# Performance work log

Measured on AMD Instinct MI355X. Metric: run time of the kernel, lower is better.

Reference implementation:

```python
import jax, jax.numpy as jnp
import numpy as np

B, S, D = 4, 2048, 1024
H = 16
HD = D // H          # 64
HALF = HD // 2       # 32


def _rope(t, cos, sin):
    # t: [B, S, H, HD]; cos/sin: [S, HALF]
    tr = t.reshape(*t.shape[:-1], HALF, 2)
    t0, t1 = tr[..., 0], tr[..., 1]
    c = cos[None, :, None, :]
    s = sin[None, :, None, :]
    out = jnp.stack([t0 * c - t1 * s, t0 * s + t1 * c], axis=-1)
    return out.reshape(t.shape)


def setup_inputs() -> dict:
    key = jax.random.key(0)
    ks = jax.random.split(key, 7)
    x = jax.random.normal(ks[0], (B, S, D), dtype=jnp.float32)
    # rotary tables (theta=10000 convention)
    inv_freq = 1.0 / (10000.0 ** (np.arange(0, HD, 2, dtype=np.float32) / HD))
    angles = np.arange(S, dtype=np.float32)[:, None] * inv_freq[None, :]
    freqs_cos = jnp.asarray(np.cos(angles))
    freqs_sin = jnp.asarray(np.sin(angles))
    scale = 1.0 / np.sqrt(D)
    wq = jax.random.normal(ks[1], (D, D), dtype=jnp.float32) * scale
    wk = jax.random.normal(ks[2], (D, D), dtype=jnp.float32) * scale
    wv = jax.random.normal(ks[3], (D, D), dtype=jnp.float32) * scale
    wo = jax.random.normal(ks[4], (D, D), dtype=jnp.float32) * scale
    return {"x": x, "freqs_cos": freqs_cos, "freqs_sin": freqs_sin,
            "wq": wq, "wk": wk, "wv": wv, "wo": wo}


def reference(x, freqs_cos, freqs_sin, wq, wk, wv, wo):
    b, s, d = x.shape
    q = (x @ wq.T).reshape(b, s, H, HD)
    k = (x @ wk.T).reshape(b, s, H, HD)
    v = (x @ wv.T).reshape(b, s, H, HD)
    q = _rope(q, freqs_cos, freqs_sin)
    k = _rope(k, freqs_cos, freqs_sin)
    # [B, H, S, HD]
    q = q.transpose(0, 2, 1, 3)
    k = k.transpose(0, 2, 1, 3)
    v = v.transpose(0, 2, 1, 3)
    scores = jnp.einsum("bhqd,bhkd->bhqk", q, k) / jnp.sqrt(jnp.float32(HD))
    causal = jnp.tril(jnp.ones((s, s), dtype=bool))
    scores = jnp.where(causal[None, None, :, :], scores, jnp.finfo(scores.dtype).min)
    attn = jax.nn.softmax(scores, axis=-1)
    out = jnp.einsum("bhqk,bhkd->bhqd", attn, v)
    out = out.transpose(0, 2, 1, 3).reshape(b, s, d)
    return out @ wo.T
```

## Files before the change

### kernel.cpp

```cpp
#include <hip/hip_runtime.h>
#include <hip/hip_bf16.h>
#include <cstdint>
#include <cstddef>

#define BB 4
#define SS 2048
#define DD 1024
#define HH 16
#define HDD 64

typedef __bf16 bf16_t;
typedef __bf16 bf16x8 __attribute__((ext_vector_type(8)));
typedef float f32x4 __attribute__((ext_vector_type(4)));
typedef unsigned u32x2 __attribute__((ext_vector_type(2)));

__device__ __forceinline__ unsigned short f2bf(float f) {
    unsigned u = __float_as_uint(f);
    unsigned r = (u + 0x7FFFu + ((u >> 16) & 1u)) >> 16;
    return (unsigned short)r;
}
__device__ __forceinline__ bf16_t f2bf16(float f) {
    return __builtin_bit_cast(bf16_t, f2bf(f));
}
__device__ __forceinline__ bf16x8 cvt8(float4 a, float4 b) {
    bf16x8 r;
    r[0] = f2bf16(a.x); r[1] = f2bf16(a.y);
    r[2] = f2bf16(a.z); r[3] = f2bf16(a.w);
    r[4] = f2bf16(b.x); r[5] = f2bf16(b.y);
    r[6] = f2bf16(b.z); r[7] = f2bf16(b.w);
    return r;
}
__device__ __forceinline__ unsigned cvtpk_bf16(float lo, float hi) {
    unsigned r;
    asm("v_cvt_pk_bf16_f32 %0, %1, %2" : "=v"(r) : "v"(lo), "v"(hi));
    return r;
}
__device__ __forceinline__ float exp2_raw(float x) {
    float r;
    asm("v_exp_f32 %0, %1" : "=v"(r) : "v"(x));
    return r;
}

#define GLL16(gp, lp)                                                          \
    __builtin_amdgcn_global_load_lds(                                          \
        (const __attribute__((address_space(1))) void*)(gp),                   \
        (__attribute__((address_space(3))) void*)(lp), 16, 0, 0)

__global__ __launch_bounds__(256) void cvt1(const float* __restrict__ in,
                                            bf16_t* __restrict__ out) {
    size_t i = (size_t)blockIdx.x * 256 + threadIdx.x;
    const float4* p = (const float4*)in + i * 2;
    *(bf16x8*)(out + i * 8) = cvt8(p[0], p[1]);
}
__global__ __launch_bounds__(256) void cvt4(
    const float* __restrict__ w0, const float* __restrict__ w1,
    const float* __restrict__ w2, const float* __restrict__ w3,
    bf16_t* __restrict__ o0, bf16_t* __restrict__ o1,
    bf16_t* __restrict__ o2, bf16_t* __restrict__ o3) {
    const float* in = blockIdx.y == 0 ? w0 : blockIdx.y == 1 ? w1
                    : blockIdx.y == 2 ? w2 : w3;
    bf16_t* out = blockIdx.y == 0 ? o0 : blockIdx.y == 1 ? o1
                : blockIdx.y == 2 ? o2 : o3;
    size_t i = (size_t)blockIdx.x * 256 + threadIdx.x;
    const float4* p = (const float4*)in + i * 2;
    *(bf16x8*)(out + i * 8) = cvt8(p[0], p[1]);
}

__global__ __launch_bounds__(256, 2) void gemm_qkv(
    const bf16_t* __restrict__ A, const bf16_t* __restrict__ Wall,
    bf16_t* __restrict__ Qb, bf16_t* __restrict__ Kb,
    bf16_t* __restrict__ Vt,
    const float* __restrict__ fcos, const float* __restrict__ fsin,
    float qscale)
{
    constexpr int K = 1024;
    __shared__ alignas(16) bf16_t lA[128 * 64];
    __shared__ alignas(16) bf16_t lB[128 * 64];

    const int tid  = threadIdx.x;
    const int w    = tid >> 6;
    const int lane = tid & 63;
    const int quad = lane >> 4;
    const int l16  = lane & 15;
    const int wm   = w >> 1;
    const int wn   = w & 1;
    const int m0   = blockIdx.y * 128;
    const int n0   = blockIdx.x * 128;
    const int sub  = n0 >> 10;

    f32x4 acc[4][4];
#pragma unroll
    for (int i = 0; i < 4; i++)
#pragma unroll
        for (int j = 0; j < 4; j++) acc[i][j] = (f32x4){0.f, 0.f, 0.f, 0.f};

    const int srow8 = lane >> 3;
    const int slot  = lane & 7;

    for (int k0 = 0; k0 < K; k0 += 64) {
#pragma unroll
        for (int i = 0; i < 4; ++i) {
            int row = w * 32 + i * 8;
            GLL16(A + (size_t)(m0 + row + srow8) * K + k0 + slot * 8,
                  &lA[row * 64]);
            GLL16(Wall + (size_t)(n0 + row + srow8) * K + k0 + slot * 8,
                  &lB[row * 64]);
        }
        __syncthreads();
#pragma unroll
        for (int kk = 0; kk < 2; ++kk) {
            bf16x8 af[4], bfr[4];
#pragma unroll
            for (int mt = 0; mt < 4; ++mt)
                af[mt] = *(const bf16x8*)
                    &lA[(wm * 64 + mt * 16 + l16) * 64 + (kk * 4 + quad) * 8];
#pragma unroll
            for (int nt = 0; nt < 4; ++nt)
                bfr[nt] = *(const bf16x8*)
                    &lB[(wn * 64 + nt * 16 + l16) * 64 + (kk * 4 + quad) * 8];
#pragma unroll
            for (int mt = 0; mt < 4; ++mt)
#pragma unroll
                for (int nt = 0; nt < 4; ++nt)
                    acc[mt][nt] = __builtin_amdgcn_mfma_f32_16x16x32_bf16(
                        af[mt], bfr[nt], acc[mt][nt], 0, 0, 0);
        }
        __syncthreads();
    }

    if (sub < 2) {
        unsigned short* Cu = (unsigned short*)(sub == 0 ? Qb : Kb);
        const float scale = sub == 0 ? qscale : 1.0f;
#pragma unroll
        for (int mt = 0; mt < 4; ++mt) {
#pragma unroll
            for (int nt = 0; nt < 4; ++nt) {
                int col  = (n0 & 1023) + wn * 64 + nt * 16 + l16;
                int h    = col >> 6;
                int d    = col & 63;
                int pidx = d >> 1;
                bool even = (col & 1) == 0;
#pragma unroll
                for (int r = 0; r < 4; ++r) {
                    int m = m0 + wm * 64 + mt * 16 + quad * 4 + r;
                    int b = m >> 11;
                    int s = m & 2047;
                    float v  = acc[mt][nt][r];
                    float p  = __shfl_xor(v, 1);
                    float c  = fcos[s * 32 + pidx];
                    float sn = fsin[s * 32 + pidx];
                    float o  = even ? (v * c - p * sn) : (p * sn + v * c);
                    Cu[(size_t)((b * HH + h) * SS + s) * HDD + d] =
                        f2bf(o * scale);
                }
            }
        }
    } else {
        unsigned short* Cu = (unsigned short*)Vt;
#pragma unroll
        for (int mt = 0; mt < 4; ++mt) {
#pragma unroll
            for (int nt = 0; nt < 4; ++nt) {
                int col = (n0 & 1023) + wn * 64 + nt * 16 + l16;
                int h = col >> 6, d = col & 63;
#pragma unroll
                for (int r = 0; r < 4; ++r) {
                    int m = m0 + wm * 64 + mt * 16 + quad * 4 + r;
                    int b = m >> 11, s = m & 2047;
                    Cu[(size_t)((b * HH + h) * HDD + d) * SS + s] =
                        f2bf(acc[mt][nt][r]);
                }
            }
        }
    }
}

__global__ __launch_bounds__(256, 2) void gemm_out(
    const bf16_t* __restrict__ A, const bf16_t* __restrict__ W,
    float* __restrict__ Cf)
{
    constexpr int K = 1024, N = 1024;
    __shared__ alignas(16) bf16_t lA[128 * 64];
    __shared__ alignas(16) bf16_t lB[128 * 64];

    const int tid  = threadIdx.x;
    const int w    = tid >> 6;
    const int lane = tid & 63;
    const int quad = lane >> 4;
    const int l16  = lane & 15;
    const int wm   = w >> 1;
    const int wn   = w & 1;
    const int m0   = blockIdx.y * 128;
    const int n0   = blockIdx.x * 128;

    f32x4 acc[4][4];
#pragma unroll
    for (int i = 0; i < 4; i++)
#pragma unroll
        for (int j = 0; j < 4; j++) acc[i][j] = (f32x4){0.f, 0.f, 0.f, 0.f};

    const int srow8 = lane >> 3;
    const int slot  = lane & 7;

    for (int k0 = 0; k0 < K; k0 += 64) {
#pragma unroll
        for (int i = 0; i < 4; ++i) {
            int row = w * 32 + i * 8;
            GLL16(A + (size_t)(m0 + row + srow8) * K + k0 + slot * 8,
                  &lA[row * 64]);
            GLL16(W + (size_t)(n0 + row + srow8) * K + k0 + slot * 8,
                  &lB[row * 64]);
        }
        __syncthreads();
#pragma unroll
        for (int kk = 0; kk < 2; ++kk) {
            bf16x8 af[4], bfr[4];
#pragma unroll
            for (int mt = 0; mt < 4; ++mt)
                af[mt] = *(const bf16x8*)
                    &lA[(wm * 64 + mt * 16 + l16) * 64 + (kk * 4 + quad) * 8];
#pragma unroll
            for (int nt = 0; nt < 4; ++nt)
                bfr[nt] = *(const bf16x8*)
                    &lB[(wn * 64 + nt * 16 + l16) * 64 + (kk * 4 + quad) * 8];
#pragma unroll
            for (int mt = 0; mt < 4; ++mt)
#pragma unroll
                for (int nt = 0; nt < 4; ++nt)
                    acc[mt][nt] = __builtin_amdgcn_mfma_f32_16x16x32_bf16(
                        af[mt], bfr[nt], acc[mt][nt], 0, 0, 0);
        }
        __syncthreads();
    }

#pragma unroll
    for (int mt = 0; mt < 4; ++mt) {
        int mrow = m0 + wm * 64 + mt * 16 + quad * 4;
#pragma unroll
        for (int nt = 0; nt < 4; ++nt) {
            int col = n0 + wn * 64 + nt * 16 + l16;
#pragma unroll
            for (int r = 0; r < 4; ++r)
                Cf[(size_t)(mrow + r) * N + col] = acc[mt][nt][r];
        }
    }
}

__global__ __launch_bounds__(256, 2) void attn(
    const bf16_t* __restrict__ Q, const bf16_t* __restrict__ Kt,
    const bf16_t* __restrict__ Vt, bf16_t* __restrict__ O)
{
    __shared__ alignas(16) bf16_t lK[64 * 64];
    __shared__ alignas(16) bf16_t lV[64 * 64];

    const int tid  = threadIdx.x;
    const int w    = tid >> 6;
    const int lane = tid & 63;
    const int quad = lane >> 4;
    const int l16  = lane & 15;

    const int blk  = blockIdx.x;
    const int xcd  = blk & 7;
    const int rest = blk >> 3;
    const int j    = rest & 15;
    const int bh   = ((rest >> 4) << 3) | xcd;
    const int T    = (j & 1) ? (j >> 1) : (15 - (j >> 1));

    const int b = bh >> 4, h = bh & 15;
    unsigned short* Ou = (unsigned short*)O;
    const bf16_t* Qb = Q  + (size_t)bh * SS * HDD;
    const bf16_t* Kb = Kt + (size_t)bh * SS * HDD;
    const bf16_t* Vb = Vt + (size_t)bh * HDD * SS;

    const int r0a = w * 16;
    const int r0b = w * 16 + 8;
    const int rra = r0a + (lane >> 3);
    const int rrb = r0b + (lane >> 3);
    const int sca = ((lane & 7) ^ (rra & 7)) * 8;
    const int scb = ((lane & 7) ^ (rrb & 7)) * 8;

    const int q0  = T * 128 + w * 32;
    const int nkb = 2 * T + 2;

    bf16x8 qf[2][2];
#pragma unroll
    for (int qs = 0; qs < 2; ++qs) {
        const bf16_t* qp =
            Qb + (size_t)(q0 + qs * 16 + l16) * HDD + quad * 8;
        qf[qs][0] = *(const bf16x8*)(qp);
        qf[qs][1] = *(const bf16x8*)(qp + 32);
    }

    f32x4 o[2][4];
    float ps[2];
#pragma unroll
    for (int qs = 0; qs < 2; ++qs) {
        ps[qs] = 0.f;
#pragma unroll
        for (int i = 0; i < 4; ++i) o[qs][i] = (f32x4){0.f, 0.f, 0.f, 0.f};
    }

    for (int ib = 0; ib < nkb; ++ib) {
        const int kb = ib * 64;

        GLL16(Kb + (size_t)(kb + rra) * HDD + sca, &lK[r0a * 64]);
        GLL16(Kb + (size_t)(kb + rrb) * HDD + scb, &lK[r0b * 64]);
        GLL16(Vb + (size_t)rra * SS + kb + sca,    &lV[r0a * 64]);
        GLL16(Vb + (size_t)rrb * SS + kb + scb,    &lV[r0b * 64]);
        __syncthreads();

        if (kb < q0 + 32) {
            const bool diag = (kb + 63 > q0);

            bf16x8 kf[4][2];
#pragma unroll
            for (int nt = 0; nt < 4; ++nt) {
                const int row = nt * 16 + l16;
#pragma unroll
                for (int hf = 0; hf < 2; ++hf)
                    kf[nt][hf] = *(const bf16x8*)
                        &lK[row * 64 + (((hf * 4 + quad) ^ (row & 7)) * 8)];
            }
            bf16x8 vf[2][4];
#pragma unroll
            for (int kk = 0; kk < 2; ++kk)
#pragma unroll
                for (int nt = 0; nt < 4; ++nt) {
                    const int row = nt * 16 + l16;
                    vf[kk][nt] = *(const bf16x8*)
                        &lV[row * 64 + (((kk * 4 + quad) ^ (row & 7)) * 8)];
                }

            unsigned pk[4][2][2];
#pragma unroll
            for (int nt = 0; nt < 4; ++nt) {
                const int krow = kb + nt * 16 + quad * 4;
#pragma unroll
                for (int qs = 0; qs < 2; ++qs) {
                    f32x4 s = (f32x4){0.f, 0.f, 0.f, 0.f};
                    s = __builtin_amdgcn_mfma_f32_16x16x32_bf16(
                        kf[nt][0], qf[qs][0], s, 0, 0, 0);
                    s = __builtin_amdgcn_mfma_f32_16x16x32_bf16(
                        kf[nt][1], qf[qs][1], s, 0, 0, 0);
                    if (diag) {
                        const int qcol = q0 + qs * 16 + l16;
#pragma unroll
                        for (int r = 0; r < 4; ++r)
                            if (krow + r > qcol) s[r] = -1e30f;
                    }
                    float ev[4];
#pragma unroll
                    for (int r = 0; r < 4; ++r) {
                        float e = exp2_raw(s[r]);
                        ps[qs] += e;
                        ev[r] = e;
                    }
                    pk[nt][qs][0] = cvtpk_bf16(ev[0], ev[1]);
                    pk[nt][qs][1] = cvtpk_bf16(ev[2], ev[3]);
                }
            }

#pragma unroll
            for (int kk = 0; kk < 2; ++kk) {
#pragma unroll
                for (int qs = 0; qs < 2; ++qs) {
                    u32x2 sA = __builtin_amdgcn_permlane32_swap(
                        pk[2 * kk][qs][0], pk[2 * kk + 1][qs][0],
                        false, false);
                    u32x2 sB = __builtin_amdgcn_permlane32_swap(
                        pk[2 * kk][qs][1], pk[2 * kk + 1][qs][1],
                        false, false);
                    u32x2 tA = __builtin_amdgcn_permlane16_swap(
                        sA.x, sA.y, false, false);
                    u32x2 tB = __builtin_amdgcn_permlane16_swap(
                        sB.x, sB.y, false, false);
                    union { unsigned d[4]; bf16x8 v; } pf;
                    pf.d[0] = tA.x;
                    pf.d[1] = tB.x;
                    pf.d[2] = tA.y;
                    pf.d[3] = tB.y;
#pragma unroll
                    for (int nt = 0; nt < 4; ++nt)
                        o[qs][nt] = __builtin_amdgcn_mfma_f32_16x16x32_bf16(
                            pf.v, vf[kk][nt], o[qs][nt], 0, 0, 0);
                }
            }
        }
        __syncthreads();
    }

#pragma unroll
    for (int qs = 0; qs < 2; ++qs) {
        float tsum = ps[qs];
        tsum += __shfl_xor(tsum, 16);
        tsum += __shfl_xor(tsum, 32);
        float inv[4];
#pragma unroll
        for (int r = 0; r < 4; ++r)
            inv[r] = 1.0f / __shfl(tsum, quad * 4 + r);
#pragma unroll
        for (int nt = 0; nt < 4; ++nt) {
            int d = nt * 16 + l16;
#pragma unroll
            for (int r = 0; r < 4; ++r) {
                int s = q0 + qs * 16 + quad * 4 + r;
                Ou[(size_t)(b * SS + s) * DD + h * HDD + d] =
                    f2bf(o[qs][nt][r] * inv[r]);
            }
        }
    }
}

extern "C" void kernel_launch(void* const* d_in, const int* in_sizes, int n_in,
                              void* d_out, int out_size, void* d_ws,
                              size_t ws_size, hipStream_t stream)
{
    const float* x    = (const float*)d_in[0];
    const float* fcos = (const float*)d_in[1];
    const float* fsin = (const float*)d_in[2];
    const float* wq   = (const float*)d_in[3];
    const float* wk   = (const float*)d_in[4];
    const float* wv   = (const float*)d_in[5];
    const float* wo   = (const float*)d_in[6];

    char* ws = (char*)d_ws;
    const size_t TSZ = (size_t)BB * SS * DD * sizeof(bf16_t);
    const size_t WSZ = (size_t)DD * DD * sizeof(bf16_t);
    bf16_t* Qb  = (bf16_t*)(ws);
    bf16_t* Kb  = (bf16_t*)(ws + TSZ);
    bf16_t* Ob  = (bf16_t*)(ws + 2 * TSZ);
    bf16_t* wb0 = (bf16_t*)(ws + 3 * TSZ);
    bf16_t* wb1 = (bf16_t*)(ws + 3 * TSZ + WSZ);
    bf16_t* wb2 = (bf16_t*)(ws + 3 * TSZ + 2 * WSZ);
    bf16_t* wb3 = (bf16_t*)(ws + 3 * TSZ + 3 * WSZ);
    bf16_t* xb  = (bf16_t*)d_out;
    bf16_t* Vt  = (bf16_t*)((char*)d_out + TSZ);

    dim3 bb(256);
    cvt1<<<dim3(4096), bb, 0, stream>>>(x, xb);
    cvt4<<<dim3(512, 4), bb, 0, stream>>>(wq, wk, wv, wo, wb0, wb1, wb2, wb3);

    const float sscale = 0.125f * 1.44269504088896f;
    gemm_qkv<<<dim3(24, 64), bb, 0, stream>>>(xb, wb0, Qb, Kb, Vt,
                                              fcos, fsin, sscale);
    attn<<<dim3(1024), bb, 0, stream>>>(Qb, Kb, Vt, Ob);
    gemm_out<<<dim3(8, 64), bb, 0, stream>>>(Ob, wb3, (float*)d_out);
}
```

Baseline: 276.8 us.

## Double-buffer LDS tiles in output GEMM and attention K/V loops

Measured after the change: 279.8 us. About the same (+1.1%).

```diff
diff --git a/kernel.cpp b/kernel.cpp
--- a/kernel.cpp
+++ b/kernel.cpp
@@ -180,8 +180,8 @@
     float* __restrict__ Cf)
 {
     constexpr int K = 1024, N = 1024;
-    __shared__ alignas(16) bf16_t lA[128 * 64];
-    __shared__ alignas(16) bf16_t lB[128 * 64];
+    __shared__ alignas(16) bf16_t lA[2][128 * 64];
+    __shared__ alignas(16) bf16_t lB[2][128 * 64];
 
     const int tid  = threadIdx.x;
     const int w    = tid >> 6;
@@ -202,27 +202,34 @@
     const int srow8 = lane >> 3;
     const int slot  = lane & 7;
 
-    for (int k0 = 0; k0 < K; k0 += 64) {
+    auto stage = [&](int k0, int buf) {
 #pragma unroll
         for (int i = 0; i < 4; ++i) {
             int row = w * 32 + i * 8;
             GLL16(A + (size_t)(m0 + row + srow8) * K + k0 + slot * 8,
-                  &lA[row * 64]);
+                  &lA[buf][row * 64]);
             GLL16(W + (size_t)(n0 + row + srow8) * K + k0 + slot * 8,
-                  &lB[row * 64]);
-        }
-        __syncthreads();
+                  &lB[buf][row * 64]);
+        }
+    };
+
+    stage(0, 0);
+    __syncthreads();
+
+    int cur = 0;
+    for (int k0 = 0; k0 < K; k0 += 64, cur ^= 1) {
+        if (k0 + 64 < K) stage(k0 + 64, cur ^ 1);
 #pragma unroll
         for (int kk = 0; kk < 2; ++kk) {
             bf16x8 af[4], bfr[4];
 #pragma unroll
             for (int mt = 0; mt < 4; ++mt)
                 af[mt] = *(const bf16x8*)
-                    &lA[(wm * 64 + mt * 16 + l16) * 64 + (kk * 4 + quad) * 8];
+                    &lA[cur][(wm * 64 + mt * 16 + l16) * 64 + (kk * 4 + quad) * 8];
 #pragma unroll
             for (int nt = 0; nt < 4; ++nt)
                 bfr[nt] = *(const bf16x8*)
-                    &lB[(wn * 64 + nt * 16 + l16) * 64 + (kk * 4 + quad) * 8];
+                    &lB[cur][(wn * 64 + nt * 16 + l16) * 64 + (kk * 4 + quad) * 8];
 #pragma unroll
             for (int mt = 0; mt < 4; ++mt)
 #pragma unroll
@@ -250,8 +257,8 @@
     const bf16_t* __restrict__ Q, const bf16_t* __restrict__ Kt,
     const bf16_t* __restrict__ Vt, bf16_t* __restrict__ O)
 {
-    __shared__ alignas(16) bf16_t lK[64 * 64];
-    __shared__ alignas(16) bf16_t lV[64 * 64];
+    __shared__ alignas(16) bf16_t lK[2][64 * 64];
+    __shared__ alignas(16) bf16_t lV[2][64 * 64];
 
     const int tid  = threadIdx.x;
     const int w    = tid >> 6;
@@ -282,6 +289,13 @@
     const int q0  = T * 128 + w * 32;
     const int nkb = 2 * T + 2;
 
+    auto stage = [&](int kb, int buf) {
+        GLL16(Kb + (size_t)(kb + rra) * HDD + sca, &lK[buf][r0a * 64]);
+        GLL16(Kb + (size_t)(kb + rrb) * HDD + scb, &lK[buf][r0b * 64]);
+        GLL16(Vb + (size_t)rra * SS + kb + sca,    &lV[buf][r0a * 64]);
+        GLL16(Vb + (size_t)rrb * SS + kb + scb,    &lV[buf][r0b * 64]);
+    };
+
     bf16x8 qf[2][2];
 #pragma unroll
     for (int qs = 0; qs < 2; ++qs) {
@@ -300,14 +314,14 @@
         for (int i = 0; i < 4; ++i) o[qs][i] = (f32x4){0.f, 0.f, 0.f, 0.f};
     }
 
+    stage(0, 0);
+    __syncthreads();
+
     for (int ib = 0; ib < nkb; ++ib) {
-        const int kb = ib * 64;
-
-        GLL16(Kb + (size_t)(kb + rra) * HDD + sca, &lK[r0a * 64]);
-        GLL16(Kb + (size_t)(kb + rrb) * HDD + scb, &lK[r0b * 64]);
-        GLL16(Vb + (size_t)rra * SS + kb + sca,    &lV[r0a * 64]);
-        GLL16(Vb + (size_t)rrb * SS + kb + scb,    &lV[r0b * 64]);
-        __syncthreads();
+        const int kb  = ib * 64;
+        const int cur = ib & 1;
+
+        if (ib + 1 < nkb) stage(kb + 64, cur ^ 1);
 
         if (kb < q0 + 32) {
             const bool diag = (kb + 63 > q0);
@@ -319,7 +333,7 @@
 #pragma unroll
                 for (int hf = 0; hf < 2; ++hf)
                     kf[nt][hf] = *(const bf16x8*)
-                        &lK[row * 64 + (((hf * 4 + quad) ^ (row & 7)) * 8)];
+                        &lK[cur][row * 64 + (((hf * 4 + quad) ^ (row & 7)) * 8)];
             }
             bf16x8 vf[2][4];
 #pragma unroll
@@ -328,7 +342,7 @@
                 for (int nt = 0; nt < 4; ++nt) {
                     const int row = nt * 16 + l16;
                     vf[kk][nt] = *(const bf16x8*)
-                        &lV[row * 64 + (((kk * 4 + quad) ^ (row & 7)) * 8)];
+                        &lV[cur][row * 64 + (((kk * 4 + quad) ^ (row & 7)) * 8)];
                 }
 
             unsigned pk[4][2][2];
```
